# Kernel tuning notes

Hardware: AMD Instinct MI355X
Metric: run time of the kernel (lower is better)

## Reference

```python
import jax, jax.numpy as jnp
import numpy as np
from math import sqrt

L_LAYERS = 4
VOCAB = 32000
D = 1024
H = 16
HD = D // H
FFN = 4096
B = 4
LT = 1024
LS = 1024
NEG = -1e9
EPS = 1e-6


def rms_norm(x, g):
    ms = jnp.mean(x * x, axis=-1, keepdims=True)
    return x / jnp.sqrt(ms + EPS) * g


def attention(q_in, kv_in, wq, wk, wv, wo, mask=None):
    # q_in: [B,Lq,D], kv_in: [B,Lk,D]; weights [D,D]
    Bq, Lq, _ = q_in.shape
    Lk = kv_in.shape[1]
    q = (q_in @ wq).reshape(Bq, Lq, H, HD).transpose(0, 2, 1, 3)
    k = (kv_in @ wk).reshape(Bq, Lk, H, HD).transpose(0, 2, 1, 3)
    v = (kv_in @ wv).reshape(Bq, Lk, H, HD).transpose(0, 2, 1, 3)
    scores = jnp.einsum('bhqd,bhkd->bhqk', q, k) / sqrt(HD)
    if mask is not None:
        scores = scores + mask  # [Lq,Lk] broadcast
    attn = jax.nn.softmax(scores, axis=-1)
    out = jnp.einsum('bhqk,bhkd->bhqd', attn, v)
    out = out.transpose(0, 2, 1, 3).reshape(Bq, Lq, D)
    return out @ wo


def setup_inputs() -> dict:
    key = jax.random.key(0)
    ks = jax.random.split(key, 20)
    s = 0.02
    inp = {
        'input_ids': jax.random.randint(ks[0], (B, LT), 0, VOCAB),
        'memory': jax.random.normal(ks[1], (B, LS, D), dtype=jnp.float32),
        'embed': jax.random.normal(ks[2], (VOCAB, D), dtype=jnp.float32) * s,
        'sa_g': jnp.ones((L_LAYERS, D), dtype=jnp.float32),
        'sa_wq': jax.random.normal(ks[3], (L_LAYERS, D, D), dtype=jnp.float32) * s,
        'sa_wk': jax.random.normal(ks[4], (L_LAYERS, D, D), dtype=jnp.float32) * s,
        'sa_wv': jax.random.normal(ks[5], (L_LAYERS, D, D), dtype=jnp.float32) * s,
        'sa_wo': jax.random.normal(ks[6], (L_LAYERS, D, D), dtype=jnp.float32) * s,
        'ca_g': jnp.ones((L_LAYERS, D), dtype=jnp.float32),
        'ca_wq': jax.random.normal(ks[7], (L_LAYERS, D, D), dtype=jnp.float32) * s,
        'ca_wk': jax.random.normal(ks[8], (L_LAYERS, D, D), dtype=jnp.float32) * s,
        'ca_wv': jax.random.normal(ks[9], (L_LAYERS, D, D), dtype=jnp.float32) * s,
        'ca_wo': jax.random.normal(ks[10], (L_LAYERS, D, D), dtype=jnp.float32) * s,
        'mlp_g': jnp.ones((L_LAYERS, D), dtype=jnp.float32),
        'w1': jax.random.normal(ks[11], (L_LAYERS, D, FFN), dtype=jnp.float32) * s,
        'w2': jax.random.normal(ks[12], (L_LAYERS, FFN, D), dtype=jnp.float32) * s,
        'final_g': jnp.ones((D,), dtype=jnp.float32),
    }
    return inp


def reference(input_ids, memory, embed, sa_g, sa_wq, sa_wk, sa_wv, sa_wo,
              ca_g, ca_wq, ca_wk, ca_wv, ca_wo, mlp_g, w1, w2, final_g):
    Lt = input_ids.shape[1]
    causal = jnp.where(jnp.triu(jnp.ones((Lt, Lt), dtype=bool), k=1), NEG, 0.0).astype(jnp.float32)
    x = embed[input_ids]  # [B,Lt,D]
    for i in range(L_LAYERS):
        h = rms_norm(x, sa_g[i])
        x = x + attention(h, h, sa_wq[i], sa_wk[i], sa_wv[i], sa_wo[i], mask=causal)
        h = rms_norm(x, ca_g[i])
        x = x + attention(h, memory, ca_wq[i], ca_wk[i], ca_wv[i], ca_wo[i])
        h = rms_norm(x, mlp_g[i])
        x = x + jax.nn.relu(h @ w1[i]) @ w2[i]
    return rms_norm(x, final_g)
```

## Files before the change

### kernel.cpp

```cpp
#include <hip/hip_runtime.h>
#include <stdint.h>

#define NLAYERS 4
#define D      1024
#define H      16
#define HD     64
#define FFN    4096
#define BATCH  4
#define LT     1024
#define LS     1024
#define BT     (BATCH*LT)

typedef unsigned short u16;
typedef long long ll;

typedef short  short8 __attribute__((ext_vector_type(8)));
typedef float  f32x4  __attribute__((ext_vector_type(4)));

typedef __attribute__((address_space(1))) void as1_void;
typedef __attribute__((address_space(3))) void as3_void;

__device__ __forceinline__ float bf2f(u16 u) {
    unsigned int x = ((unsigned int)u) << 16;
    return __builtin_bit_cast(float, x);
}
__device__ __forceinline__ u16 f2bf(float f) {
    unsigned int x = __builtin_bit_cast(unsigned int, f);
    x += 0x7fffu + ((x >> 16) & 1u);
    return (u16)(x >> 16);
}

__device__ __forceinline__ void load16_to_lds(const void* g, void* l) {
    __builtin_amdgcn_global_load_lds((as1_void*)(void*)g, (as3_void*)l, 16, 0, 0);
}

__global__ void probe_kernel(const unsigned int* __restrict__ g, int* __restrict__ flag)
{
    if (threadIdx.x == 0) *flag = (*g == 0x3F803F80u) ? 0 : 1;
}

__global__ __launch_bounds__(256) void gemm_bt(
    const u16* __restrict__ A, const u16* __restrict__ Bt,
    void* __restrict__ Cout,
    int K, int lda, int ldb, int ldc,
    ll strideA, ll strideB, ll strideC,
    int Nvalid, int mode)
{
    __shared__ u16 sA[128 * 32];
    __shared__ u16 sB[128 * 32];

    const int tid  = threadIdx.x;
    const int wave = tid >> 6;
    const int lane = tid & 63;
    const int wm   = wave >> 1;
    const int wn   = wave & 1;
    const int quad = lane >> 4;
    const int l16  = lane & 15;
    const int bm = blockIdx.y, bn = blockIdx.x;
    const ll  z  = blockIdx.z;

    const u16* Ab = A + z * strideA;
    const u16* Bb = Bt + z * strideB;

    f32x4 acc[4][4];
#pragma unroll
    for (int i = 0; i < 4; ++i)
#pragma unroll
        for (int j = 0; j < 4; ++j) acc[i][j] = (f32x4){0.f, 0.f, 0.f, 0.f};

    const int i0 = wave * 64 + lane;
    const int i1 = 256 + i0;
    const int rA0 = i0 >> 2, ke0 = (i0 & 3) * 8;
    const int rA1 = i1 >> 2, ke1 = (i1 & 3) * 8;
    u16* lA0 = &sA[(wave * 64) * 8];
    u16* lA1 = &sA[(256 + wave * 64) * 8];
    u16* lB0 = &sB[(wave * 64) * 8];
    u16* lB1 = &sB[(256 + wave * 64) * 8];

    const u16* gA0 = Ab + (ll)(bm * 128 + rA0) * lda + ke0;
    const u16* gA1 = Ab + (ll)(bm * 128 + rA1) * lda + ke1;
    const u16* gB0 = Bb + (ll)(bn * 128 + rA0) * ldb + ke0;
    const u16* gB1 = Bb + (ll)(bn * 128 + rA1) * ldb + ke1;

    for (int kt = 0; kt < K; kt += 32) {
        __syncthreads();
        load16_to_lds(gA0 + kt, lA0);
        load16_to_lds(gA1 + kt, lA1);
        load16_to_lds(gB0 + kt, lB0);
        load16_to_lds(gB1 + kt, lB1);
        __syncthreads();

        short8 af[4], bfv[4];
#pragma unroll
        for (int mi = 0; mi < 4; ++mi) {
            int r = wm * 64 + mi * 16 + l16;
            af[mi] = *(const short8*)&sA[r * 32 + quad * 8];
        }
#pragma unroll
        for (int ni = 0; ni < 4; ++ni) {
            int n = wn * 64 + ni * 16 + l16;
            bfv[ni] = *(const short8*)&sB[n * 32 + quad * 8];
        }
#pragma unroll
        for (int mi = 0; mi < 4; ++mi)
#pragma unroll
            for (int ni = 0; ni < 4; ++ni)
                acc[mi][ni] = __builtin_amdgcn_mfma_f32_16x16x32_bf16(
                    af[mi], bfv[ni], acc[mi][ni], 0, 0, 0);
    }

    if (mode == 3) {
        float* O = (float*)Cout;
#pragma unroll
        for (int mi = 0; mi < 4; ++mi) {
#pragma unroll
            for (int r = 0; r < 4; ++r) {
                int row = bm * 128 + wm * 64 + mi * 16 + quad * 4 + r;
                ll base = z * strideC + (ll)row * ldc;
#pragma unroll
                for (int ni = 0; ni < 4; ++ni) {
                    int col = bn * 128 + wn * 64 + ni * 16 + l16;
                    if (col < Nvalid) atomicAdd(&O[base + col], acc[mi][ni][r]);
                }
            }
        }
    } else {
        u16* O = (u16*)Cout;
#pragma unroll
        for (int mi = 0; mi < 4; ++mi) {
#pragma unroll
            for (int r = 0; r < 4; ++r) {
                int row = bm * 128 + wm * 64 + mi * 16 + quad * 4 + r;
                ll base = z * strideC + (ll)row * ldc;
#pragma unroll
                for (int ni = 0; ni < 4; ++ni) {
                    int col = bn * 128 + wn * 64 + ni * 16 + l16;
                    if (col < Nvalid) {
                        float v = acc[mi][ni][r];
                        if (mode == 1) v = fmaxf(v, 0.f);
                        O[base + col] = f2bf(v);
                    }
                }
            }
        }
    }
}

#define FA_PAD 132

__global__ __launch_bounds__(256, 3) void flash_attn(
    const u16* __restrict__ Qp, int q_ld,
    const u16* __restrict__ Kp, int k_ld,
    const u16* __restrict__ Vt,
    u16* __restrict__ Op, int o_ld, int causal)
{
    __shared__ u16 uni[128 * FA_PAD];
    __shared__ u16 sV[4 * 64 * 32];

    u16* sK = uni;
    u16* sP = uni;

    const int tid  = threadIdx.x;
    const int wave = tid >> 6, lane = tid & 63;
    const int quad = lane >> 4, l16 = lane & 15;
    const int rw   = wave * 32;
    const int bm = blockIdx.x;
    const int z  = blockIdx.y;
    const int b = z >> 4, h = z & 15;

    const u16* Qb = Qp + (ll)(b * LT) * q_ld + h * HD;
    const u16* Kb = Kp + (ll)(b * LS) * k_ld + h * HD;
    const u16* Vb = Vt + (ll)z * HD * LS;

#pragma unroll
    for (int j = 0; j < 4; ++j) {
        int i = wave * 256 + j * 64 + lane;
        int ks = i >> 9, n = (i >> 2) & 127, c = i & 3;
        load16_to_lds(Qb + (ll)(bm * 128 + n) * q_ld + ks * 32 + c * 8,
                      (char*)uni + (wave * 256 + j * 64) * 16);
    }
    __syncthreads();
    short8 afq[2][2];
#pragma unroll
    for (int mi = 0; mi < 2; ++mi)
#pragma unroll
        for (int ks = 0; ks < 2; ++ks)
            afq[mi][ks] = *(const short8*)&uni[ks * 4096 + (rw + mi * 16 + l16) * 32 + quad * 8];
    __syncthreads();

    float m_s[2][4];
    f32x4 Oacc[2][4], Ol[2];
#pragma unroll
    for (int mi = 0; mi < 2; ++mi) {
#pragma unroll
        for (int r = 0; r < 4; ++r) m_s[mi][r] = -1e30f;
#pragma unroll
        for (int di = 0; di < 4; ++di) Oacc[mi][di] = (f32x4){0.f, 0.f, 0.f, 0.f};
        Ol[mi] = (f32x4){0.f, 0.f, 0.f, 0.f};
    }
    const float c1 = 0.1803368801111204f;
    short8 ones;
#pragma unroll
    for (int i = 0; i < 8; ++i) ones[i] = (short)0x3F80;

    const int n_kt = causal ? (bm + 1) : (LS / 128);

    for (int kt = 0; kt < n_kt; ++kt) {
#pragma unroll
        for (int j = 0; j < 4; ++j) {
            int i = wave * 256 + j * 64 + lane;
            int ks = i >> 9, n = (i >> 2) & 127, c = i & 3;
            load16_to_lds(Kb + (ll)(kt * 128 + n) * k_ld + ks * 32 + c * 8,
                          (char*)sK + (wave * 256 + j * 64) * 16);
        }
#pragma unroll
        for (int j = 0; j < 4; ++j) {
            int i = wave * 256 + j * 64 + lane;
            int kk = i >> 8, d = (i >> 2) & 63, c = i & 3;
            load16_to_lds(Vb + (ll)d * LS + kt * 128 + kk * 32 + c * 8,
                          (char*)sV + (wave * 256 + j * 64) * 16);
        }
        __syncthreads();

        f32x4 s[2][8];
#pragma unroll
        for (int mi = 0; mi < 2; ++mi)
#pragma unroll
            for (int ni = 0; ni < 8; ++ni) s[mi][ni] = (f32x4){0.f, 0.f, 0.f, 0.f};
#pragma unroll
        for (int ks = 0; ks < 2; ++ks)
#pragma unroll
            for (int nh = 0; nh < 2; ++nh) {
                short8 bk[4];
#pragma unroll
                for (int nn = 0; nn < 4; ++nn)
                    bk[nn] = *(const short8*)&sK[ks * 4096 + ((nh * 4 + nn) * 16 + l16) * 32 + quad * 8];
#pragma unroll
                for (int mi = 0; mi < 2; ++mi)
#pragma unroll
                    for (int nn = 0; nn < 4; ++nn)
                        s[mi][nh * 4 + nn] = __builtin_amdgcn_mfma_f32_16x16x32_bf16(
                            afq[mi][ks], bk[nn], s[mi][nh * 4 + nn], 0, 0, 0);
            }
        __syncthreads();

        const int diag = causal && (kt == bm);
        float pm[2][4];
#pragma unroll
        for (int mi = 0; mi < 2; ++mi)
#pragma unroll
            for (int r = 0; r < 4; ++r) pm[mi][r] = -1e30f;
#pragma unroll
        for (int mi = 0; mi < 2; ++mi)
#pragma unroll
            for (int ni = 0; ni < 8; ++ni)
#pragma unroll
                for (int r = 0; r < 4; ++r) {
                    float t = s[mi][ni][r] * c1;
                    if (diag) {
                        int rowg = rw + mi * 16 + quad * 4 + r;
                        int colg = ni * 16 + l16;
                        if (colg > rowg) t = -1e30f;
                    }
                    s[mi][ni][r] = t;
                    pm[mi][r] = fmaxf(pm[mi][r], t);
                }
#pragma unroll
        for (int off = 1; off < 16; off <<= 1)
#pragma unroll
            for (int mi = 0; mi < 2; ++mi)
#pragma unroll
                for (int r = 0; r < 4; ++r)
                    pm[mi][r] = fmaxf(pm[mi][r], __shfl_xor(pm[mi][r], off));

        float alpha[2][4];
#pragma unroll
        for (int mi = 0; mi < 2; ++mi)
#pragma unroll
            for (int r = 0; r < 4; ++r) {
                float mnew = fmaxf(m_s[mi][r], pm[mi][r]);
                alpha[mi][r] = __builtin_amdgcn_exp2f(m_s[mi][r] - mnew);
                m_s[mi][r] = mnew;
            }
#pragma unroll
        for (int mi = 0; mi < 2; ++mi)
#pragma unroll
            for (int r = 0; r < 4; ++r) {
#pragma unroll
                for (int di = 0; di < 4; ++di) Oacc[mi][di][r] *= alpha[mi][r];
                Ol[mi][r] *= alpha[mi][r];
            }

#pragma unroll
        for (int mi = 0; mi < 2; ++mi)
#pragma unroll
            for (int ni = 0; ni < 8; ++ni)
#pragma unroll
                for (int r = 0; r < 4; ++r) {
                    float pv = __builtin_amdgcn_exp2f(s[mi][ni][r] - m_s[mi][r]);
                    sP[(rw + mi * 16 + quad * 4 + r) * FA_PAD + ni * 16 + l16] = f2bf(pv);
                }

#pragma unroll
        for (int kk = 0; kk < 4; ++kk) {
            short8 ap[2], bv[4];
#pragma unroll
            for (int mi = 0; mi < 2; ++mi)
                ap[mi] = *(const short8*)&sP[(rw + mi * 16 + l16) * FA_PAD + kk * 32 + quad * 8];
#pragma unroll
            for (int di = 0; di < 4; ++di)
                bv[di] = *(const short8*)&sV[kk * 2048 + (di * 16 + l16) * 32 + quad * 8];
#pragma unroll
            for (int mi = 0; mi < 2; ++mi) {
#pragma unroll
                for (int di = 0; di < 4; ++di)
                    Oacc[mi][di] = __builtin_amdgcn_mfma_f32_16x16x32_bf16(
                        ap[mi], bv[di], Oacc[mi][di], 0, 0, 0);
                Ol[mi] = __builtin_amdgcn_mfma_f32_16x16x32_bf16(
                    ap[mi], ones, Ol[mi], 0, 0, 0);
            }
        }
        __syncthreads();
    }

#pragma unroll
    for (int mi = 0; mi < 2; ++mi)
#pragma unroll
        for (int di = 0; di < 4; ++di)
#pragma unroll
            for (int r = 0; r < 4; ++r) {
                int rowg = bm * 128 + rw + mi * 16 + quad * 4 + r;
                int col  = h * HD + di * 16 + l16;
                Op[(ll)(b * LT + rowg) * o_ld + col] = f2bf(Oacc[mi][di][r] / Ol[mi][r]);
            }
}

__global__ __launch_bounds__(256) void transpose_any(
    const void* __restrict__ inb, ll elem_off, u16* __restrict__ out,
    int in_stride, int out_stride, const int* __restrict__ flagp)
{
    __shared__ u16 t[32][33];
    const int fl = *flagp;
    int bk = blockIdx.x * 32;
    int bn = blockIdx.y * 32;
    int c  = threadIdx.x & 31;
    int r0 = threadIdx.x >> 5;
#pragma unroll
    for (int i = 0; i < 4; ++i) {
        int r = r0 + i * 8;
        ll idx = elem_off + (ll)(bk + r) * in_stride + bn + c;
        t[r][c] = fl ? f2bf(((const float*)inb)[idx]) : ((const u16*)inb)[idx];
    }
    __syncthreads();
#pragma unroll
    for (int i = 0; i < 4; ++i) {
        int r = r0 + i * 8;
        out[(ll)(bn + r) * out_stride + bk + c] = t[c][r];
    }
}

__global__ __launch_bounds__(256) void trans3_kernel(
    const void* __restrict__ s0, const void* __restrict__ s1, const void* __restrict__ s2,
    ll elem_off, u16* __restrict__ dst, const int* __restrict__ flagp)
{
    __shared__ u16 t[32][33];
    const int fl = *flagp;
    int zz = blockIdx.z;
    const void* src = (zz == 0) ? s0 : (zz == 1) ? s1 : s2;
    u16* out = dst + (ll)zz * D * D;
    int bk = blockIdx.x * 32, bn = blockIdx.y * 32;
    int c = threadIdx.x & 31, r0 = threadIdx.x >> 5;
#pragma unroll
    for (int i = 0; i < 4; ++i) {
        int r = r0 + i * 8;
        ll idx = elem_off + (ll)(bk + r) * D + bn + c;
        t[r][c] = fl ? f2bf(((const float*)src)[idx]) : ((const u16*)src)[idx];
    }
    __syncthreads();
#pragma unroll
    for (int i = 0; i < 4; ++i) {
        int r = r0 + i * 8;
        out[(ll)(bn + r) * D + bk + c] = t[c][r];
    }
}

__global__ __launch_bounds__(256) void transpose_v_kernel(
    const u16* __restrict__ V, int v_ld, u16* __restrict__ Vt)
{
    __shared__ u16 t[32][33];
    int z = blockIdx.z;
    int b = z >> 4, h = z & 15;
    const u16* in = V + (ll)b * LT * v_ld + h * HD;
    u16* out = Vt + (ll)z * HD * LS;
    int bt = blockIdx.x * 32;
    int bd = blockIdx.y * 32;
    int c  = threadIdx.x & 31;
    int r0 = threadIdx.x >> 5;
#pragma unroll
    for (int i = 0; i < 4; ++i) {
        int r = r0 + i * 8;
        t[r][c] = in[(ll)(bt + r) * v_ld + bd + c];
    }
    __syncthreads();
#pragma unroll
    for (int i = 0; i < 4; ++i) {
        int r = r0 + i * 8;
        out[(ll)(bd + r) * LS + bt + c] = t[c][r];
    }
}

__global__ __launch_bounds__(256) void convert_memory(
    const void* __restrict__ mem, u16* __restrict__ out, const int* __restrict__ flagp)
{
    const int fl = *flagp;
    ll i = (ll)blockIdx.x * 1024 + threadIdx.x * 4;
#pragma unroll
    for (int j = 0; j < 4; ++j)
        out[i + j] = fl ? f2bf(((const float*)mem)[i + j]) : ((const u16*)mem)[i + j];
}

__global__ __launch_bounds__(256) void embed_kernel(
    const int* __restrict__ ids, const void* __restrict__ emb, float* __restrict__ x,
    const int* __restrict__ flagp)
{
    const int fl = *flagp;
    ll row = blockIdx.x;
    int id = ids[row];
    float* xr = x + row * D;
    int j = threadIdx.x * 4;
#pragma unroll
    for (int i = 0; i < 4; ++i) {
        ll idx = (ll)id * D + j + i;
        xr[j + i] = fl ? ((const float*)emb)[idx] : bf2f(((const u16*)emb)[idx]);
    }
}

__global__ __launch_bounds__(256) void rmsnorm_kernel(
    const float* __restrict__ x, const void* __restrict__ gb, ll g_off,
    void* __restrict__ out, const int* __restrict__ flagp, int is_final)
{
    __shared__ float red[4];
    const int fl = *flagp;
    ll row = blockIdx.x;
    const float* xr = x + row * D;
    int tid = threadIdx.x;
    float4 v = ((const float4*)xr)[tid];
    float s = v.x * v.x + v.y * v.y + v.z * v.z + v.w * v.w;
#pragma unroll
    for (int o = 32; o; o >>= 1) s += __shfl_xor(s, o);
    if ((tid & 63) == 0) red[tid >> 6] = s;
    __syncthreads();
    s = red[0] + red[1] + red[2] + red[3];
    float inv = rsqrtf(s * (1.0f / D) + 1e-6f);
    int j = tid * 4;
    float e[4] = {v.x, v.y, v.z, v.w};
#pragma unroll
    for (int i = 0; i < 4; ++i) {
        ll gi = g_off + j + i;
        float g = fl ? ((const float*)gb)[gi] : bf2f(((const u16*)gb)[gi]);
        float val = e[i] * inv * g;
        if (is_final && fl) ((float*)out)[row * D + j + i] = val;
        else                ((u16*)out)[row * D + j + i] = f2bf(val);
    }
}

extern "C" void kernel_launch(void* const* d_in, const int* in_sizes, int n_in,
                              void* d_out, int out_size, void* d_ws, size_t ws_size,
                              hipStream_t stream)
{
    (void)in_sizes; (void)n_in; (void)out_size; (void)ws_size;

    const int*  ids    = (const int*)d_in[0];
    const void* memory = d_in[1];
    const void* embed  = d_in[2];
    const void* sa_g   = d_in[3];
    const void* sa_wq  = d_in[4];
    const void* sa_wk  = d_in[5];
    const void* sa_wv  = d_in[6];
    const void* sa_wo  = d_in[7];
    const void* ca_g   = d_in[8];
    const void* ca_wq  = d_in[9];
    const void* ca_wk  = d_in[10];
    const void* ca_wv  = d_in[11];
    const void* ca_wo  = d_in[12];
    const void* mlp_g  = d_in[13];
    const void* w1     = d_in[14];
    const void* w2     = d_in[15];
    const void* final_g= d_in[16];

    char* p = (char*)d_ws;
    auto alloc = [&](size_t bytes) -> void* {
        void* r = (void*)p;
        p += (bytes + 255) & ~(size_t)255;
        return r;
    };
    int*   flag   = (int*)alloc(256);
    u16*   wt_qkv = (u16*)alloc((size_t)3 * D * D * 2);
    u16*   wt_q   = wt_qkv;
    u16*   wt_kv  = wt_qkv + (size_t)D * D;
    u16*   wt_o   = (u16*)alloc((size_t)D * D * 2);
    u16*   wt1    = (u16*)alloc((size_t)FFN * D * 2);
    u16*   wt2    = (u16*)alloc((size_t)D * FFN * 2);
    float* x      = (float*)alloc((size_t)BT * D * 4);
    u16*   h      = (u16*)alloc((size_t)BT * D * 2);
    u16*   memb   = (u16*)alloc((size_t)BT * D * 2);
    u16*   vt     = (u16*)alloc((size_t)BATCH * H * HD * LS * 2);
    u16*   ob     = (u16*)alloc((size_t)BT * D * 2);
    u16*   smid   = (u16*)alloc((size_t)BT * FFN * 2);
    u16*   qkvb   = smid;
    u16*   mid    = smid;

    probe_kernel<<<1, 64, 0, stream>>>((const unsigned int*)final_g, flag);

    auto gemm = [&](const u16* A, const u16* Bt, void* C,
                    int M, int Npad, int K, int lda, int ldb, int ldc,
                    ll sA, ll sB, ll sC, int batch, int mode) {
        dim3 grid(Npad / 128, M / 128, batch);
        gemm_bt<<<grid, 256, 0, stream>>>(A, Bt, C, K, lda, ldb, ldc,
                                          sA, sB, sC, Npad, mode);
    };

    embed_kernel<<<BT, 256, 0, stream>>>(ids, embed, x, flag);
    convert_memory<<<BT * D / 1024, 256, 0, stream>>>(memory, memb, flag);

    for (int il = 0; il < NLAYERS; ++il) {
        const ll wOff = (ll)il * D * D;

        trans3_kernel<<<dim3(D/32, D/32, 3), 256, 0, stream>>>(
            sa_wq, sa_wk, sa_wv, wOff, wt_qkv, flag);
        transpose_any<<<dim3(D/32, D/32), 256, 0, stream>>>(sa_wo, wOff, wt_o, D, D, flag);
        rmsnorm_kernel<<<BT, 256, 0, stream>>>(x, sa_g, (ll)il * D, h, flag, 0);
        gemm(h, wt_qkv, qkvb, BT, 3 * D, D, D, D, 3 * D, 0, 0, 0, 1, 0);
        transpose_v_kernel<<<dim3(LT/32, HD/32, BATCH*H), 256, 0, stream>>>(qkvb + 2 * D, 3 * D, vt);
        flash_attn<<<dim3(LT/128, BATCH*H), 256, 0, stream>>>(
            qkvb, 3 * D, qkvb + D, 3 * D, vt, ob, D, 1);
        gemm(ob, wt_o, x, BT, D, 256, D, D, D, 256, 256, 0, 4, 3);

        trans3_kernel<<<dim3(D/32, D/32, 3), 256, 0, stream>>>(
            ca_wq, ca_wk, ca_wv, wOff, wt_qkv, flag);
        transpose_any<<<dim3(D/32, D/32), 256, 0, stream>>>(ca_wo, wOff, wt_o, D, D, flag);
        rmsnorm_kernel<<<BT, 256, 0, stream>>>(x, ca_g, (ll)il * D, h, flag, 0);
        gemm(h, wt_q, qkvb, BT, D, D, D, D, 3 * D, 0, 0, 0, 1, 0);
        gemm(memb, wt_kv, qkvb + D, BT, 2 * D, D, D, D, 3 * D, 0, 0, 0, 1, 0);
        transpose_v_kernel<<<dim3(LT/32, HD/32, BATCH*H), 256, 0, stream>>>(qkvb + 2 * D, 3 * D, vt);
        flash_attn<<<dim3(LT/128, BATCH*H), 256, 0, stream>>>(
            qkvb, 3 * D, qkvb + D, 3 * D, vt, ob, D, 0);
        gemm(ob, wt_o, x, BT, D, 256, D, D, D, 256, 256, 0, 4, 3);

        transpose_any<<<dim3(D/32, FFN/32), 256, 0, stream>>>(w1, (ll)il * D * FFN, wt1, FFN, D, flag);
        transpose_any<<<dim3(FFN/32, D/32), 256, 0, stream>>>(w2, (ll)il * FFN * D, wt2, D, FFN, flag);
        rmsnorm_kernel<<<BT, 256, 0, stream>>>(x, mlp_g, (ll)il * D, h, flag, 0);
        gemm(h, wt1, mid, BT, FFN, D, D, D, FFN, 0, 0, 0, 1, 1);
        gemm(mid, wt2, x, BT, D, 1024, FFN, FFN, D, 1024, 1024, 0, 4, 3);
    }

    rmsnorm_kernel<<<BT, 256, 0, stream>>>(x, final_g, 0, d_out, flag, 1);
}
```

Measured before the change: 2.719 ms.

## Replace split-K atomic accumulation with partial buffers reduced in fused rmsnorm

The split-K output-projection and FFN-down GEMMs now write their fp32 partial sums to separate slices of a scratch buffer with plain stores, instead of doing atomicAdd into the residual. The following rmsnorm kernel adds the partial slices into the residual, writes the updated residual back, and normalizes in the same pass. Attention output projections now use 2 K-splits instead of 4. This removes atomic contention and read-modify-write traffic, at the cost of extra partial-buffer writes and reads and less split-K parallelism for the attention projections.

After: 2.412 ms. 1.13x faster.

```diff
diff --git a/kernel.cpp b/kernel.cpp
--- a/kernel.cpp
+++ b/kernel.cpp
@@ -109,7 +109,7 @@
                     af[mi], bfv[ni], acc[mi][ni], 0, 0, 0);
     }
 
-    if (mode == 3) {
+    if (mode == 4) {
         float* O = (float*)Cout;
 #pragma unroll
         for (int mi = 0; mi < 4; ++mi) {
@@ -120,7 +120,7 @@
 #pragma unroll
                 for (int ni = 0; ni < 4; ++ni) {
                     int col = bn * 128 + wn * 64 + ni * 16 + l16;
-                    if (col < Nvalid) atomicAdd(&O[base + col], acc[mi][ni][r]);
+                    if (col < Nvalid) O[base + col] = acc[mi][ni][r];
                 }
             }
         }
@@ -435,16 +435,22 @@
     }
 }
 
-__global__ __launch_bounds__(256) void rmsnorm_kernel(
-    const float* __restrict__ x, const void* __restrict__ gb, ll g_off,
+__global__ __launch_bounds__(256) void rmsnorm_fused(
+    float* __restrict__ x, const float* __restrict__ P, int nP,
+    const void* __restrict__ gb, ll g_off,
     void* __restrict__ out, const int* __restrict__ flagp, int is_final)
 {
     __shared__ float red[4];
     const int fl = *flagp;
     ll row = blockIdx.x;
-    const float* xr = x + row * D;
+    float* xr = x + row * D;
     int tid = threadIdx.x;
     float4 v = ((const float4*)xr)[tid];
+    for (int zz = 0; zz < nP; ++zz) {
+        float4 pv = ((const float4*)(P + ((ll)zz * BT + row) * D))[tid];
+        v.x += pv.x; v.y += pv.y; v.z += pv.z; v.w += pv.w;
+    }
+    if (nP && !is_final) ((float4*)xr)[tid] = v;
     float s = v.x * v.x + v.y * v.y + v.z * v.z + v.w * v.w;
 #pragma unroll
     for (int o = 32; o; o >>= 1) s += __shfl_xor(s, o);
@@ -506,6 +512,7 @@
     u16*   memb   = (u16*)alloc((size_t)BT * D * 2);
     u16*   vt     = (u16*)alloc((size_t)BATCH * H * HD * LS * 2);
     u16*   ob     = (u16*)alloc((size_t)BT * D * 2);
+    float* Pp     = (float*)alloc((size_t)4 * BT * D * 4);
     u16*   smid   = (u16*)alloc((size_t)BT * FFN * 2);
     u16*   qkvb   = smid;
     u16*   mid    = smid;
@@ -519,40 +526,47 @@
         gemm_bt<<<grid, 256, 0, stream>>>(A, Bt, C, K, lda, ldb, ldc,
                                           sA, sB, sC, Npad, mode);
     };
+    auto rms = [&](const float* Ppart, int nP, const void* g, ll g_off,
+                   void* out, int is_final) {
+        rmsnorm_fused<<<BT, 256, 0, stream>>>((float*)x, Ppart, nP, g, g_off,
+                                              out, flag, is_final);
+    };
 
     embed_kernel<<<BT, 256, 0, stream>>>(ids, embed, x, flag);
     convert_memory<<<BT * D / 1024, 256, 0, stream>>>(memory, memb, flag);
 
+    int pend = 0;
     for (int il = 0; il < NLAYERS; ++il) {
         const ll wOff = (ll)il * D * D;
 
         trans3_kernel<<<dim3(D/32, D/32, 3), 256, 0, stream>>>(
             sa_wq, sa_wk, sa_wv, wOff, wt_qkv, flag);
         transpose_any<<<dim3(D/32, D/32), 256, 0, stream>>>(sa_wo, wOff, wt_o, D, D, flag);
-        rmsnorm_kernel<<<BT, 256, 0, stream>>>(x, sa_g, (ll)il * D, h, flag, 0);
+        rms(Pp, pend, sa_g, (ll)il * D, h, 0);
         gemm(h, wt_qkv, qkvb, BT, 3 * D, D, D, D, 3 * D, 0, 0, 0, 1, 0);
         transpose_v_kernel<<<dim3(LT/32, HD/32, BATCH*H), 256, 0, stream>>>(qkvb + 2 * D, 3 * D, vt);
         flash_attn<<<dim3(LT/128, BATCH*H), 256, 0, stream>>>(
             qkvb, 3 * D, qkvb + D, 3 * D, vt, ob, D, 1);
-        gemm(ob, wt_o, x, BT, D, 256, D, D, D, 256, 256, 0, 4, 3);
+        gemm(ob, wt_o, Pp, BT, D, 512, D, D, D, 512, 512, (ll)BT * D, 2, 4);
 
         trans3_kernel<<<dim3(D/32, D/32, 3), 256, 0, stream>>>(
             ca_wq, ca_wk, ca_wv, wOff, wt_qkv, flag);
         transpose_any<<<dim3(D/32, D/32), 256, 0, stream>>>(ca_wo, wOff, wt_o, D, D, flag);
-        rmsnorm_kernel<<<BT, 256, 0, stream>>>(x, ca_g, (ll)il * D, h, flag, 0);
+        rms(Pp, 2, ca_g, (ll)il * D, h, 0);
         gemm(h, wt_q, qkvb, BT, D, D, D, D, 3 * D, 0, 0, 0, 1, 0);
         gemm(memb, wt_kv, qkvb + D, BT, 2 * D, D, D, D, 3 * D, 0, 0, 0, 1, 0);
         transpose_v_kernel<<<dim3(LT/32, HD/32, BATCH*H), 256, 0, stream>>>(qkvb + 2 * D, 3 * D, vt);
         flash_attn<<<dim3(LT/128, BATCH*H), 256, 0, stream>>>(
             qkvb, 3 * D, qkvb + D, 3 * D, vt, ob, D, 0);
-        gemm(ob, wt_o, x, BT, D, 256, D, D, D, 256, 256, 0, 4, 3);
+        gemm(ob, wt_o, Pp, BT, D, 512, D, D, D, 512, 512, (ll)BT * D, 2, 4);
 
         transpose_any<<<dim3(D/32, FFN/32), 256, 0, stream>>>(w1, (ll)il * D * FFN, wt1, FFN, D, flag);
         transpose_any<<<dim3(FFN/32, D/32), 256, 0, stream>>>(w2, (ll)il * FFN * D, wt2, D, FFN, flag);
-        rmsnorm_kernel<<<BT, 256, 0, stream>>>(x, mlp_g, (ll)il * D, h, flag, 0);
+        rms(Pp, 2, mlp_g, (ll)il * D, h, 0);
         gemm(h, wt1, mid, BT, FFN, D, D, D, FFN, 0, 0, 0, 1, 1);
-        gemm(mid, wt2, x, BT, D, 1024, FFN, FFN, D, 1024, 1024, 0, 4, 3);
-    }
-
-    rmsnorm_kernel<<<BT, 256, 0, stream>>>(x, final_g, 0, d_out, flag, 1);
-}
+        gemm(mid, wt2, Pp, BT, D, 1024, FFN, FFN, D, 1024, 1024, (ll)BT * D, 4, 4);
+        pend = 4;
+    }
+
+    rms(Pp, 4, final_g, 0, d_out, 1);
+}
```
